# Performance work log

Hardware: AMD Instinct MI355X
Metric: run time of the kernel (lower is better)

## Reference

```python
import jax, jax.numpy as jnp
import numpy as np

N_NODES = 100000
N_EDGES = 1600000
F_IN = 128
HID = 128
N_CLASSES = 10
N_GRAPHS = 128
N_LAYERS = 4


def _uniform(key, shape, fan_in):
    s = 1.0 / np.sqrt(fan_in)
    return jax.random.uniform(key, shape, jnp.float32, -s, s)


def setup_inputs() -> dict:
    key = jax.random.key(0)
    ks = jax.random.split(key, 14)
    x = jax.random.normal(ks[0], (N_NODES, F_IN), jnp.float32)
    edge_index = jax.random.randint(ks[1], (2, N_EDGES), 0, N_NODES, dtype=jnp.int32)
    batch = jnp.sort(jax.random.randint(ks[2], (N_NODES,), 0, N_GRAPHS, dtype=jnp.int32))
    # GraphConv layer 1: lin_rel (with bias) + lin_root (no bias)
    W1_rel = _uniform(ks[3], (F_IN, HID), F_IN)
    b1_rel = _uniform(ks[4], (HID,), F_IN)
    W1_root = _uniform(ks[5], (F_IN, HID), F_IN)
    # remaining num_layers-1 GraphConv layers, stacked
    Wc_rel = _uniform(ks[6], (N_LAYERS - 1, HID, HID), HID)
    bc_rel = _uniform(ks[7], (N_LAYERS - 1, HID), HID)
    Wc_root = _uniform(ks[8], (N_LAYERS - 1, HID, HID), HID)
    # JumpingKnowledge 'cat' -> lin1: (num_layers*hidden) -> hidden
    Wl1 = _uniform(ks[9], (N_LAYERS * HID, HID), N_LAYERS * HID)
    bl1 = _uniform(ks[10], (HID,), N_LAYERS * HID)
    Wl2 = _uniform(ks[11], (HID, N_CLASSES), HID)
    bl2 = _uniform(ks[12], (N_CLASSES,), HID)
    return {
        "x": x, "edge_index": edge_index, "batch": batch,
        "W1_rel": W1_rel, "b1_rel": b1_rel, "W1_root": W1_root,
        "Wc_rel": Wc_rel, "bc_rel": bc_rel, "Wc_root": Wc_root,
        "Wl1": Wl1, "bl1": bl1, "Wl2": Wl2, "bl2": bl2,
    }


def reference(x, edge_index, batch, W1_rel, b1_rel, W1_root,
              Wc_rel, bc_rel, Wc_root, Wl1, bl1, Wl2, bl2):
    src, dst = edge_index[0], edge_index[1]

    def graph_conv(h, Wr, br, Wroot):
        # GraphConv (aggr='add'): lin_rel(sum_{j in N(i)} x_j) + lin_root(x_i)
        agg = jax.ops.segment_sum(h[src], dst, num_segments=N_NODES)
        return agg @ Wr + br + h @ Wroot

    counts = jax.ops.segment_sum(jnp.ones((N_NODES, 1), x.dtype), batch,
                                 num_segments=N_GRAPHS)
    counts = jnp.maximum(counts, 1.0)

    def global_mean_pool(h):
        sums = jax.ops.segment_sum(h, batch, num_segments=N_GRAPHS)
        return sums / counts

    h = jax.nn.relu(graph_conv(x, W1_rel, b1_rel, W1_root))
    xs = [global_mean_pool(h)]
    for i in range(N_LAYERS - 1):
        h = jax.nn.relu(graph_conv(h, Wc_rel[i], bc_rel[i], Wc_root[i]))
        xs.append(global_mean_pool(h))

    z = jnp.concatenate(xs, axis=-1)            # [N_GRAPHS, N_LAYERS*HID]
    z = jax.nn.relu(z @ Wl1 + bl1)
    return z @ Wl2 + bl2                        # [N_GRAPHS, N_CLASSES]
```

## Files before the change

### kernel.cpp

```cpp
#include <hip/hip_runtime.h>

#define NNODES 100000
#define NEDGES 1600000
#define FDIM 128
#define NGRAPHS 128
#define NLAYERS 4
#define NCLASS 10
#define LDC 136
#define LDC8 136
#define NBUCK 391
#define EBCAP 5120
#define EPB 4096
#define NBLK_E ((NEDGES + EPB - 1) / EPB)

typedef __attribute__((ext_vector_type(8))) short bf16x8;
typedef __attribute__((ext_vector_type(4))) float f32x4;
typedef __attribute__((ext_vector_type(2))) float f32x2;
typedef unsigned char u8;
typedef unsigned short u16;
typedef unsigned int u32;
typedef unsigned long long u64;

__device__ __forceinline__ u16 f2bf(float f) {
    u32 u = __float_as_uint(f);
    u += 0x7fffu + ((u >> 16) & 1u);
    return (u16)(u >> 16);
}
__device__ __forceinline__ u32 pack_bf(float a, float b) {
    return (u32)f2bf(a) | ((u32)f2bf(b) << 16);
}

__device__ __forceinline__ void gload_lds16(const u16* g, u16* l) {
    __builtin_amdgcn_global_load_lds(
        (const __attribute__((address_space(1))) u32*)g,
        (__attribute__((address_space(3))) u32*)l, 16, 0, 0);
}


__global__ __launch_bounds__(256) void conv_x(const float* __restrict__ x,
                                              u16* __restrict__ xb,
                                              u8* __restrict__ x8) {
    int i = (blockIdx.x * 256 + threadIdx.x) * 4;
    if (i < NNODES * FDIM) {
        float4 v = *(const float4*)(x + i);
        u32 p0 = pack_bf(v.x, v.y), p1 = pack_bf(v.z, v.w);
        *(u32*)(xb + i) = p0;
        *(u32*)(xb + i + 2) = p1;
        u32 a = (u32)__builtin_amdgcn_cvt_pk_fp8_f32(v.x, v.y, 0, 0);
        u32 b = (u32)__builtin_amdgcn_cvt_pk_fp8_f32(v.z, v.w, 0, 0);
        *(u32*)(x8 + i) = (a & 0xffffu) | (b << 16);
    }
}

__global__ __launch_bounds__(256) void conv_w(const float* __restrict__ W1_rel,
                                              const float* __restrict__ W1_root,
                                              const float* __restrict__ Wc_rel,
                                              const float* __restrict__ Wc_root,
                                              u16* __restrict__ Wcat) {
    int idx = blockIdx.x * 256 + threadIdx.x;
    if (idx >= NLAYERS * 256 * FDIM) return;
    int n = idx & 127;
    int k = (idx >> 7) & 255;
    int l = idx >> 15;
    const float* Wr = (l == 0) ? W1_rel  : Wc_rel  + (size_t)(l - 1) * FDIM * FDIM;
    const float* Wt = (l == 0) ? W1_root : Wc_root + (size_t)(l - 1) * FDIM * FDIM;
    float v = (k < 128) ? Wr[(size_t)k * FDIM + n] : Wt[(size_t)(k - 128) * FDIM + n];
    Wcat[(size_t)l * 32768 + (size_t)n * 256 + k] = f2bf(v);
}


__global__ __launch_bounds__(192) void graph_ptr_kernel(const int* __restrict__ batch,
                                                        int* __restrict__ gptr) {
    int g = threadIdx.x;
    if (g > NGRAPHS) return;
    int lo = 0, hi = NNODES;
    while (lo < hi) {
        int mid = (lo + hi) >> 1;
        if (batch[mid] < g) lo = mid + 1; else hi = mid;
    }
    gptr[g] = lo;
}

__global__ __launch_bounds__(256) void bcur_init(int* __restrict__ bcur) {
    int i = blockIdx.x * 256 + threadIdx.x;
    if (i < NBUCK) bcur[i] = i * EBCAP;
}

__global__ __launch_bounds__(256) void bucket_scatter(const int* __restrict__ src,
                                                      const int* __restrict__ dst,
                                                      int* __restrict__ bcur,
                                                      u64* __restrict__ ebuf) {
    __shared__ int cnt[NBUCK];
    for (int i = threadIdx.x; i < NBUCK; i += 256) cnt[i] = 0;
    __syncthreads();
    int e0 = blockIdx.x * EPB;
    int e1 = e0 + EPB; if (e1 > NEDGES) e1 = NEDGES;
    for (int e = e0 + threadIdx.x; e < e1; e += 256)
        atomicAdd(&cnt[dst[e] >> 8], 1);
    __syncthreads();
    for (int i = threadIdx.x; i < NBUCK; i += 256) {
        int c = cnt[i];
        if (c) cnt[i] = atomicAdd(&bcur[i], c);
    }
    __syncthreads();
    for (int e = e0 + threadIdx.x; e < e1; e += 256) {
        int d = dst[e], s = src[e];
        int pos = atomicAdd(&cnt[d >> 8], 1);
        ebuf[pos] = ((u64)(u32)d << 32) | (u32)s;
    }
}

__global__ __launch_bounds__(256) void bucket_csr(const u64* __restrict__ ebuf,
                                                  const int* __restrict__ bcur,
                                                  int* __restrict__ rowstart,
                                                  int* __restrict__ rowend,
                                                  int* __restrict__ csr) {
    __shared__ int cur[256];
    __shared__ int sd[256];
    int b = blockIdx.x, t = threadIdx.x;
    int ebase = b * EBCAP, eend = bcur[b];
    int n0 = b << 8;
    cur[t] = 0;
    __syncthreads();
    for (int e = ebase + t; e < eend; e += 256) {
        int d = (int)(ebuf[e] >> 32);
        atomicAdd(&cur[d & 255], 1);
    }
    __syncthreads();
    int v = cur[t];
    sd[t] = v;
    __syncthreads();
    for (int s = 1; s < 256; s <<= 1) {
        int add = (t >= s) ? sd[t - s] : 0;
        __syncthreads();
        sd[t] += add;
        __syncthreads();
    }
    int excl = sd[t] - v;
    cur[t] = ebase + excl;
    if (n0 + t < NNODES) {
        rowstart[n0 + t] = ebase + excl;
        rowend[n0 + t]   = ebase + excl + v;
    }
    __syncthreads();
    for (int e = ebase + t; e < eend; e += 256) {
        u64 r = ebuf[e];
        int d = (int)(r >> 32);
        int pos = atomicAdd(&cur[d & 255], 1);
        csr[pos] = (int)(r & 0xffffffffu);
    }
}


__global__ __launch_bounds__(256) void agg_bf(const u8* __restrict__ h8,
                                              const int* __restrict__ rowstart,
                                              const int* __restrict__ rowend,
                                              const int* __restrict__ csr,
                                              u16* __restrict__ agg) {
    int wave = threadIdx.x >> 6;
    int lane = threadIdx.x & 63;
    int node = (blockIdx.x << 2) + wave;
    if (node >= NNODES) return;
    int e0 = rowstart[node], e1 = rowend[node];
    int cnt = e1 - e0;
    float ax = 0.f, ay = 0.f;
    if (cnt <= 64) {
        int myidx = (lane < cnt) ? csr[e0 + lane] : 0;
        int nb = (cnt + 15) >> 4;
        for (int b = 0; b < nb; ++b) {
            int base = b * 16;
            u32 vv[16];
#pragma unroll
            for (int i = 0; i < 16; ++i) {
                int s = __builtin_amdgcn_readlane(myidx, base + i);
                vv[i] = *(const u16*)(h8 + (size_t)s * FDIM + lane * 2);
            }
            if (base + 16 <= cnt) {
#pragma unroll
                for (int i = 0; i < 16; ++i) {
                    f32x2 f = __builtin_amdgcn_cvt_pk_f32_fp8((int)vv[i], 0);
                    ax += f.x; ay += f.y;
                }
            } else {
#pragma unroll
                for (int i = 0; i < 16; ++i) {
                    f32x2 f = __builtin_amdgcn_cvt_pk_f32_fp8((int)vv[i], 0);
                    float m = (base + i < cnt) ? 1.f : 0.f;
                    ax = fmaf(f.x, m, ax);
                    ay = fmaf(f.y, m, ay);
                }
            }
        }
    } else {
        int e = e0;
        for (; e + 8 <= e1; e += 8) {
            u32 v0 = *(const u16*)(h8 + (size_t)csr[e]     * FDIM + lane * 2);
            u32 v1 = *(const u16*)(h8 + (size_t)csr[e + 1] * FDIM + lane * 2);
            u32 v2 = *(const u16*)(h8 + (size_t)csr[e + 2] * FDIM + lane * 2);
            u32 v3 = *(const u16*)(h8 + (size_t)csr[e + 3] * FDIM + lane * 2);
            u32 v4 = *(const u16*)(h8 + (size_t)csr[e + 4] * FDIM + lane * 2);
            u32 v5 = *(const u16*)(h8 + (size_t)csr[e + 5] * FDIM + lane * 2);
            u32 v6 = *(const u16*)(h8 + (size_t)csr[e + 6] * FDIM + lane * 2);
            u32 v7 = *(const u16*)(h8 + (size_t)csr[e + 7] * FDIM + lane * 2);
            f32x2 f0 = __builtin_amdgcn_cvt_pk_f32_fp8((int)v0, 0);
            f32x2 f1 = __builtin_amdgcn_cvt_pk_f32_fp8((int)v1, 0);
            f32x2 f2 = __builtin_amdgcn_cvt_pk_f32_fp8((int)v2, 0);
            f32x2 f3 = __builtin_amdgcn_cvt_pk_f32_fp8((int)v3, 0);
            f32x2 f4 = __builtin_amdgcn_cvt_pk_f32_fp8((int)v4, 0);
            f32x2 f5 = __builtin_amdgcn_cvt_pk_f32_fp8((int)v5, 0);
            f32x2 f6 = __builtin_amdgcn_cvt_pk_f32_fp8((int)v6, 0);
            f32x2 f7 = __builtin_amdgcn_cvt_pk_f32_fp8((int)v7, 0);
            ax += f0.x + f1.x + f2.x + f3.x + f4.x + f5.x + f6.x + f7.x;
            ay += f0.y + f1.y + f2.y + f3.y + f4.y + f5.y + f6.y + f7.y;
        }
        for (; e < e1; ++e) {
            u32 v0 = *(const u16*)(h8 + (size_t)csr[e] * FDIM + lane * 2);
            f32x2 f = __builtin_amdgcn_cvt_pk_f32_fp8((int)v0, 0);
            ax += f.x; ay += f.y;
        }
    }
    ((u32*)(agg + (size_t)node * FDIM))[lane] = pack_bf(ax, ay);
}


__global__ __launch_bounds__(256) void gemm_mfma(const u16* __restrict__ aggb,
                                                 const u16* __restrict__ hinb,
                                                 const u16* __restrict__ Wl,
                                                 const float* __restrict__ bias,
                                                 const int* __restrict__ batch,
                                                 float* __restrict__ z, int layer,
                                                 u16* __restrict__ houtb,
                                                 u8* __restrict__ hout8) {
    __shared__ u16 S[32768];
    __shared__ int batchs[128];
    u8* Cs8 = (u8*)S + 36864;
    const int t = threadIdx.x;
    const int lane = t & 63;
    const int w = t >> 6;
    const int wr = w >> 1, wc = w & 1;
    const int row0 = blockIdx.x * 128;
    const int lr = lane & 15;

    const int srow = lane >> 3;
    const int sq = lane & 7;

    auto STAGE = [&](int kb, u16* Abuf, u16* Bbuf) {
        const u16* xsrc = (kb < 2) ? aggb : hinb;
        const int koff = (kb & 1) * 64;
#pragma unroll
        for (int i = 0; i < 4; ++i) {
            int blk8 = w * 4 + i;
            int r = blk8 * 8 + srow;
            int sc = sq ^ (r & 7);
            int arow = row0 + r; if (arow > NNODES - 1) arow = NNODES - 1;
            gload_lds16(xsrc + (size_t)arow * FDIM + koff + sc * 8, Abuf + blk8 * 512);
            gload_lds16(Wl + (size_t)r * 256 + kb * 64 + sc * 8, Bbuf + blk8 * 512);
        }
    };

    f32x4 acc[4][4];
#pragma unroll
    for (int m = 0; m < 4; ++m)
#pragma unroll
        for (int n = 0; n < 4; ++n) acc[m][n] = (f32x4){0.f, 0.f, 0.f, 0.f};

    STAGE(0, S, S + 8192);
    if (t < 128) batchs[t] = (row0 + t < NNODES) ? batch[row0 + t] : NGRAPHS;
    __syncthreads();

    for (int kb = 0; kb < 4; ++kb) {
        u16* Ac = S + ((kb & 1) ? 16384 : 0);
        u16* Bc = Ac + 8192;
        if (kb < 3) {
            u16* An = S + ((kb & 1) ? 0 : 16384);
            STAGE(kb + 1, An, An + 8192);
        }
#pragma unroll
        for (int ks = 0; ks < 2; ++ks) {
            bf16x8 a[4], b[4];
            int qr = ks * 4 + (lane >> 4);
#pragma unroll
            for (int m = 0; m < 4; ++m) {
                int r = wr * 64 + m * 16 + lr;
                int ch = qr ^ (r & 7);
                a[m] = *(const bf16x8*)&Ac[r * 64 + ch * 8];
            }
#pragma unroll
            for (int n = 0; n < 4; ++n) {
                int r = wc * 64 + n * 16 + lr;
                int ch = qr ^ (r & 7);
                b[n] = *(const bf16x8*)&Bc[r * 64 + ch * 8];
            }
#pragma unroll
            for (int m = 0; m < 4; ++m)
#pragma unroll
                for (int n = 0; n < 4; ++n)
                    acc[m][n] = __builtin_amdgcn_mfma_f32_16x16x32_bf16(a[m], b[n], acc[m][n], 0, 0, 0);
        }
        __syncthreads();
    }
#pragma unroll
    for (int m = 0; m < 4; ++m) {
#pragma unroll
        for (int n = 0; n < 4; ++n) {
            int col = wc * 64 + n * 16 + lr;
            float bb = bias[col];
#pragma unroll
            for (int reg = 0; reg < 4; ++reg) {
                int row = wr * 64 + m * 16 + (lane >> 4) * 4 + reg;
                float v = fmaxf(acc[m][n][reg] + bb, 0.f);
                S[row * LDC + col] = f2bf(v);
                Cs8[row * LDC8 + col] = (u8)__builtin_amdgcn_cvt_pk_fp8_f32(v, v, 0, 0);
            }
        }
    }
    __syncthreads();
    {
        int r = t >> 1, half = t & 1;
        if (row0 + r < NNODES) {
#pragma unroll
            for (int j = 0; j < 8; ++j) {
                bf16x8 v = *(const bf16x8*)&S[r * LDC + half * 64 + j * 8];
                *(bf16x8*)(houtb + (size_t)(row0 + r) * FDIM + half * 64 + j * 8) = v;
            }
#pragma unroll
            for (int j = 0; j < 8; ++j) {
                u64 v8 = *(const u64*)&Cs8[r * LDC8 + half * 64 + j * 8];
                *(u64*)(hout8 + (size_t)(row0 + r) * FDIM + half * 64 + j * 8) = v8;
            }
        }
    }
    {
        int col = t & 127, half = t >> 7;
        int r0 = half * 64, r1 = r0 + 64;
        float* zl = z + (size_t)layer * FDIM + col;
        int g = batchs[r0];
        float s = 0.f;
        for (int r = r0; r < r1; ++r) {
            int gn = batchs[r];
            if (gn != g) {
                atomicAdd(zl + (size_t)g * (NLAYERS * FDIM), s);
                s = 0.f; g = gn;
            }
            s += __uint_as_float((u32)S[r * LDC + col] << 16);
        }
        atomicAdd(zl + (size_t)g * (NLAYERS * FDIM), s);
    }
}


__global__ __launch_bounds__(128) void mlp1(const float* __restrict__ z,
                                            const int* __restrict__ gptr,
                                            const float* __restrict__ Wl1,
                                            const float* __restrict__ bl1,
                                            float* __restrict__ z2) {
    int g = blockIdx.x, j = threadIdx.x;
    __shared__ float zs[NLAYERS * FDIM];
    int cnt = gptr[g + 1] - gptr[g]; if (cnt < 1) cnt = 1;
    float invc = 1.0f / (float)cnt;
    for (int k = j; k < NLAYERS * FDIM; k += 128)
        zs[k] = z[(size_t)g * (NLAYERS * FDIM) + k] * invc;
    __syncthreads();
    float s = bl1[j];
    for (int k = 0; k < NLAYERS * FDIM; ++k) s = fmaf(zs[k], Wl1[(size_t)k * FDIM + j], s);
    z2[(size_t)g * FDIM + j] = fmaxf(s, 0.f);
}

__global__ __launch_bounds__(128) void mlp2(const float* __restrict__ z2,
                                            const float* __restrict__ Wl2,
                                            const float* __restrict__ bl2,
                                            float* __restrict__ out) {
    int g = blockIdx.x, c = threadIdx.x;
    __shared__ float zs[FDIM];
    if (threadIdx.x < FDIM) zs[threadIdx.x] = z2[(size_t)g * FDIM + threadIdx.x];
    __syncthreads();
    if (c < NCLASS) {
        float s = bl2[c];
        for (int k = 0; k < FDIM; ++k) s = fmaf(zs[k], Wl2[(size_t)k * NCLASS + c], s);
        out[(size_t)g * NCLASS + c] = s;
    }
}


extern "C" void kernel_launch(void* const* d_in, const int* in_sizes, int n_in,
                              void* d_out, int out_size, void* d_ws, size_t ws_size,
                              hipStream_t stream) {
    const float* x       = (const float*)d_in[0];
    const int*   ei      = (const int*)d_in[1];
    const int*   batch   = (const int*)d_in[2];
    const float* W1_rel  = (const float*)d_in[3];
    const float* b1_rel  = (const float*)d_in[4];
    const float* W1_root = (const float*)d_in[5];
    const float* Wc_rel  = (const float*)d_in[6];
    const float* bc_rel  = (const float*)d_in[7];
    const float* Wc_root = (const float*)d_in[8];
    const float* Wl1     = (const float*)d_in[9];
    const float* bl1     = (const float*)d_in[10];
    const float* Wl2     = (const float*)d_in[11];
    const float* bl2     = (const float*)d_in[12];
    float* out = (float*)d_out;

    const int* srcv = ei;
    const int* dstv = ei + NEDGES;

    char* ws = (char*)d_ws;
    size_t off = 0;
    auto alloc = [&](size_t bytes) -> void* {
        void* p = ws + off;
        off = (off + bytes + 255) & ~(size_t)255;
        return p;
    };
    u16* xb      = (u16*)alloc((size_t)NNODES * FDIM * 2);
    u16* hA      = (u16*)alloc((size_t)NNODES * FDIM * 2);
    u16* hB      = (u16*)alloc((size_t)NNODES * FDIM * 2);
    u16* aggb    = (u16*)alloc((size_t)NNODES * FDIM * 2);
    u8*  x8      = (u8*)alloc((size_t)NNODES * FDIM);
    u8*  h8A     = (u8*)alloc((size_t)NNODES * FDIM);
    u8*  h8B     = (u8*)alloc((size_t)NNODES * FDIM);
    u16* Wcat    = (u16*)alloc((size_t)NLAYERS * 256 * FDIM * 2);
    int* csr     = (int*)alloc((size_t)NBUCK * EBCAP * 4);
    int* rowstart= (int*)alloc((size_t)NNODES * 4);
    int* rowend  = (int*)alloc((size_t)NNODES * 4);
    int* bcur    = (int*)alloc((size_t)(NBUCK + 1) * 4);
    int* gptr    = (int*)alloc(1024);
    float* z     = (float*)alloc((size_t)(NGRAPHS + 1) * NLAYERS * FDIM * 4);
    float* z2    = (float*)alloc((size_t)NGRAPHS * FDIM * 4);
    u64* ebuf    = (u64*)hA;
    (void)ws_size; (void)in_sizes; (void)n_in; (void)out_size;

    hipMemsetAsync(z, 0, (size_t)(NGRAPHS + 1) * NLAYERS * FDIM * 4, stream);
    conv_x<<<(NNODES * FDIM / 4 + 255) / 256, 256, 0, stream>>>(x, xb, x8);
    conv_w<<<(NLAYERS * 256 * FDIM + 255) / 256, 256, 0, stream>>>(W1_rel, W1_root, Wc_rel, Wc_root, Wcat);
    graph_ptr_kernel<<<1, 192, 0, stream>>>(batch, gptr);
    bcur_init<<<(NBUCK + 255) / 256, 256, 0, stream>>>(bcur);
    bucket_scatter<<<NBLK_E, 256, 0, stream>>>(srcv, dstv, bcur, ebuf);
    bucket_csr<<<NBUCK, 256, 0, stream>>>(ebuf, bcur, rowstart, rowend, csr);

    const u16* hin = xb;
    const u8*  hin8 = x8;
    for (int l = 0; l < NLAYERS; ++l) {
        u16* hout  = (l & 1) ? hB : hA;
        u8*  hout8 = (l & 1) ? h8B : h8A;
        const u16* Wl = Wcat + (size_t)l * 256 * FDIM;
        const float* bb = (l == 0) ? b1_rel : bc_rel + (size_t)(l - 1) * FDIM;
        agg_bf<<<(NNODES + 3) / 4, 256, 0, stream>>>(hin8, rowstart, rowend, csr, aggb);
        gemm_mfma<<<(NNODES + 127) / 128, 256, 0, stream>>>(aggb, hin, Wl, bb, batch, z, l, hout, hout8);
        hin = hout; hin8 = hout8;
    }
    mlp1<<<NGRAPHS, 128, 0, stream>>>(z, gptr, Wl1, bl1, z2);
    mlp2<<<NGRAPHS, 128, 0, stream>>>(z2, Wl2, bl2, out);
}
```

Before: 400.0 us.

## Aggregate two nodes per wave with 4-byte fp8 loads; single-buffer GEMM LDS

The neighbor aggregation kernel now gives each wave two destination nodes, one per 32-lane half. Each lane gathers 4 fp8 features with a 32-bit load and unpacks both halves, which halves the lanes spent per edge and widens each memory access. The fast path now needs both nodes to have at most 32 neighbors, and edge groups of 4 are masked by each half's own count. Separately, the MFMA GEMM drops its LDS double buffer for a single buffer with a sync after each stage, cutting shared-memory use to allow more resident blocks, at the cost of no longer overlapping loads with compute.

```diff
diff --git a/kernel.cpp b/kernel.cpp
--- a/kernel.cpp
+++ b/kernel.cpp
@@ -157,69 +157,73 @@
                                               const int* __restrict__ rowend,
                                               const int* __restrict__ csr,
                                               u16* __restrict__ agg) {
-    int wave = threadIdx.x >> 6;
-    int lane = threadIdx.x & 63;
-    int node = (blockIdx.x << 2) + wave;
-    if (node >= NNODES) return;
-    int e0 = rowstart[node], e1 = rowend[node];
-    int cnt = e1 - e0;
-    float ax = 0.f, ay = 0.f;
-    if (cnt <= 64) {
-        int myidx = (lane < cnt) ? csr[e0 + lane] : 0;
-        int nb = (cnt + 15) >> 4;
-        for (int b = 0; b < nb; ++b) {
-            int base = b * 16;
-            u32 vv[16];
-#pragma unroll
-            for (int i = 0; i < 16; ++i) {
-                int s = __builtin_amdgcn_readlane(myidx, base + i);
-                vv[i] = *(const u16*)(h8 + (size_t)s * FDIM + lane * 2);
-            }
-            if (base + 16 <= cnt) {
-#pragma unroll
-                for (int i = 0; i < 16; ++i) {
-                    f32x2 f = __builtin_amdgcn_cvt_pk_f32_fp8((int)vv[i], 0);
-                    ax += f.x; ay += f.y;
-                }
-            } else {
-#pragma unroll
-                for (int i = 0; i < 16; ++i) {
-                    f32x2 f = __builtin_amdgcn_cvt_pk_f32_fp8((int)vv[i], 0);
-                    float m = (base + i < cnt) ? 1.f : 0.f;
-                    ax = fmaf(f.x, m, ax);
-                    ay = fmaf(f.y, m, ay);
-                }
+    const int wid = threadIdx.x >> 6;
+    const int lane = threadIdx.x & 63;
+    const int half = lane >> 5;
+    const int sl = lane & 31;
+    const int pair = blockIdx.x * 4 + wid;
+    const int node = pair * 2 + half;
+    if (pair * 2 >= NNODES) return;
+
+    int e0 = rowstart[node];
+    int cnt = rowend[node] - e0;
+    float f0 = 0.f, f1 = 0.f, f2 = 0.f, f3 = 0.f;
+
+    int cA = __builtin_amdgcn_readlane(cnt, 0);
+    int cB = __builtin_amdgcn_readlane(cnt, 32);
+
+    if (cA <= 32 && cB <= 32) {
+        int myidx = (sl < cnt) ? csr[e0 + sl] : 0;
+        int cmin = cA < cB ? cA : cB;
+        int cmax = cA > cB ? cA : cB;
+        int bfull = cmin >> 2;
+        int btot = (cmax + 3) >> 2;
+        int b = 0;
+        for (; b < bfull; ++b) {
+            u32 v[4];
+#pragma unroll
+            for (int i = 0; i < 4; ++i) {
+                int iA = __builtin_amdgcn_readlane(myidx, b * 4 + i);
+                int iB = __builtin_amdgcn_readlane(myidx, 32 + b * 4 + i);
+                int s = half ? iB : iA;
+                v[i] = *(const u32*)(h8 + (size_t)s * FDIM + sl * 4);
+            }
+#pragma unroll
+            for (int i = 0; i < 4; ++i) {
+                f32x2 lo = __builtin_amdgcn_cvt_pk_f32_fp8((int)v[i], false);
+                f32x2 hi = __builtin_amdgcn_cvt_pk_f32_fp8((int)v[i], true);
+                f0 += lo.x; f1 += lo.y; f2 += hi.x; f3 += hi.y;
+            }
+        }
+        for (; b < btot; ++b) {
+            u32 v[4];
+#pragma unroll
+            for (int i = 0; i < 4; ++i) {
+                int iA = __builtin_amdgcn_readlane(myidx, b * 4 + i);
+                int iB = __builtin_amdgcn_readlane(myidx, 32 + b * 4 + i);
+                int s = half ? iB : iA;
+                v[i] = *(const u32*)(h8 + (size_t)s * FDIM + sl * 4);
+            }
+#pragma unroll
+            for (int i = 0; i < 4; ++i) {
+                float m = (b * 4 + i < cnt) ? 1.f : 0.f;
+                f32x2 lo = __builtin_amdgcn_cvt_pk_f32_fp8((int)v[i], false);
+                f32x2 hi = __builtin_amdgcn_cvt_pk_f32_fp8((int)v[i], true);
+                f0 = fmaf(lo.x, m, f0); f1 = fmaf(lo.y, m, f1);
+                f2 = fmaf(hi.x, m, f2); f3 = fmaf(hi.y, m, f3);
             }
         }
     } else {
-        int e = e0;
-        for (; e + 8 <= e1; e += 8) {
-            u32 v0 = *(const u16*)(h8 + (size_t)csr[e]     * FDIM + lane * 2);
-            u32 v1 = *(const u16*)(h8 + (size_t)csr[e + 1] * FDIM + lane * 2);
-            u32 v2 = *(const u16*)(h8 + (size_t)csr[e + 2] * FDIM + lane * 2);
-            u32 v3 = *(const u16*)(h8 + (size_t)csr[e + 3] * FDIM + lane * 2);
-            u32 v4 = *(const u16*)(h8 + (size_t)csr[e + 4] * FDIM + lane * 2);
-            u32 v5 = *(const u16*)(h8 + (size_t)csr[e + 5] * FDIM + lane * 2);
-            u32 v6 = *(const u16*)(h8 + (size_t)csr[e + 6] * FDIM + lane * 2);
-            u32 v7 = *(const u16*)(h8 + (size_t)csr[e + 7] * FDIM + lane * 2);
-            f32x2 f0 = __builtin_amdgcn_cvt_pk_f32_fp8((int)v0, 0);
-            f32x2 f1 = __builtin_amdgcn_cvt_pk_f32_fp8((int)v1, 0);
-            f32x2 f2 = __builtin_amdgcn_cvt_pk_f32_fp8((int)v2, 0);
-            f32x2 f3 = __builtin_amdgcn_cvt_pk_f32_fp8((int)v3, 0);
-            f32x2 f4 = __builtin_amdgcn_cvt_pk_f32_fp8((int)v4, 0);
-            f32x2 f5 = __builtin_amdgcn_cvt_pk_f32_fp8((int)v5, 0);
-            f32x2 f6 = __builtin_amdgcn_cvt_pk_f32_fp8((int)v6, 0);
-            f32x2 f7 = __builtin_amdgcn_cvt_pk_f32_fp8((int)v7, 0);
-            ax += f0.x + f1.x + f2.x + f3.x + f4.x + f5.x + f6.x + f7.x;
-            ay += f0.y + f1.y + f2.y + f3.y + f4.y + f5.y + f6.y + f7.y;
-        }
-        for (; e < e1; ++e) {
-            u32 v0 = *(const u16*)(h8 + (size_t)csr[e] * FDIM + lane * 2);
-            f32x2 f = __builtin_amdgcn_cvt_pk_f32_fp8((int)v0, 0);
-            ax += f.x; ay += f.y;
-        }
-    }
-    ((u32*)(agg + (size_t)node * FDIM))[lane] = pack_bf(ax, ay);
+        for (int e = 0; e < cnt; ++e) {
+            int s = csr[e0 + e];
+            u32 v = *(const u32*)(h8 + (size_t)s * FDIM + sl * 4);
+            f32x2 lo = __builtin_amdgcn_cvt_pk_f32_fp8((int)v, false);
+            f32x2 hi = __builtin_amdgcn_cvt_pk_f32_fp8((int)v, true);
+            f0 += lo.x; f1 += lo.y; f2 += hi.x; f3 += hi.y;
+        }
+    }
+    u32 p0 = pack_bf(f0, f1), p1 = pack_bf(f2, f3);
+    *(u64*)(agg + (size_t)node * FDIM + sl * 4) = ((u64)p1 << 32) | (u64)p0;
 }
 
 
@@ -231,9 +235,11 @@
                                                  float* __restrict__ z, int layer,
                                                  u16* __restrict__ houtb,
                                                  u8* __restrict__ hout8) {
-    __shared__ u16 S[32768];
+    __shared__ u16 S[26112];
     __shared__ int batchs[128];
-    u8* Cs8 = (u8*)S + 36864;
+    u16* As = S;
+    u16* Bs = S + 8192;
+    u8* Cs8 = (u8*)S + 34816;
     const int t = threadIdx.x;
     const int lane = t & 63;
     const int w = t >> 6;
@@ -244,7 +250,15 @@
     const int srow = lane >> 3;
     const int sq = lane & 7;
 
-    auto STAGE = [&](int kb, u16* Abuf, u16* Bbuf) {
+    f32x4 acc[4][4];
+#pragma unroll
+    for (int m = 0; m < 4; ++m)
+#pragma unroll
+        for (int n = 0; n < 4; ++n) acc[m][n] = (f32x4){0.f, 0.f, 0.f, 0.f};
+
+    if (t < 128) batchs[t] = (row0 + t < NNODES) ? batch[row0 + t] : NGRAPHS;
+
+    for (int kb = 0; kb < 4; ++kb) {
         const u16* xsrc = (kb < 2) ? aggb : hinb;
         const int koff = (kb & 1) * 64;
 #pragma unroll
@@ -253,28 +267,10 @@
             int r = blk8 * 8 + srow;
             int sc = sq ^ (r & 7);
             int arow = row0 + r; if (arow > NNODES - 1) arow = NNODES - 1;
-            gload_lds16(xsrc + (size_t)arow * FDIM + koff + sc * 8, Abuf + blk8 * 512);
-            gload_lds16(Wl + (size_t)r * 256 + kb * 64 + sc * 8, Bbuf + blk8 * 512);
-        }
-    };
-
-    f32x4 acc[4][4];
-#pragma unroll
-    for (int m = 0; m < 4; ++m)
-#pragma unroll
-        for (int n = 0; n < 4; ++n) acc[m][n] = (f32x4){0.f, 0.f, 0.f, 0.f};
-
-    STAGE(0, S, S + 8192);
-    if (t < 128) batchs[t] = (row0 + t < NNODES) ? batch[row0 + t] : NGRAPHS;
-    __syncthreads();
-
-    for (int kb = 0; kb < 4; ++kb) {
-        u16* Ac = S + ((kb & 1) ? 16384 : 0);
-        u16* Bc = Ac + 8192;
-        if (kb < 3) {
-            u16* An = S + ((kb & 1) ? 0 : 16384);
-            STAGE(kb + 1, An, An + 8192);
-        }
+            gload_lds16(xsrc + (size_t)arow * FDIM + koff + sc * 8, As + blk8 * 512);
+            gload_lds16(Wl + (size_t)r * 256 + kb * 64 + sc * 8, Bs + blk8 * 512);
+        }
+        __syncthreads();
 #pragma unroll
         for (int ks = 0; ks < 2; ++ks) {
             bf16x8 a[4], b[4];
@@ -283,13 +279,13 @@
             for (int m = 0; m < 4; ++m) {
                 int r = wr * 64 + m * 16 + lr;
                 int ch = qr ^ (r & 7);
-                a[m] = *(const bf16x8*)&Ac[r * 64 + ch * 8];
+                a[m] = *(const bf16x8*)&As[r * 64 + ch * 8];
             }
 #pragma unroll
             for (int n = 0; n < 4; ++n) {
                 int r = wc * 64 + n * 16 + lr;
                 int ch = qr ^ (r & 7);
-                b[n] = *(const bf16x8*)&Bc[r * 64 + ch * 8];
+                b[n] = *(const bf16x8*)&Bs[r * 64 + ch * 8];
             }
 #pragma unroll
             for (int m = 0; m < 4; ++m)
@@ -438,12 +434,13 @@
 
     const u16* hin = xb;
     const u8*  hin8 = x8;
+    const int npairs = NNODES / 2;
     for (int l = 0; l < NLAYERS; ++l) {
         u16* hout  = (l & 1) ? hB : hA;
         u8*  hout8 = (l & 1) ? h8B : h8A;
         const u16* Wl = Wcat + (size_t)l * 256 * FDIM;
         const float* bb = (l == 0) ? b1_rel : bc_rel + (size_t)(l - 1) * FDIM;
-        agg_bf<<<(NNODES + 3) / 4, 256, 0, stream>>>(hin8, rowstart, rowend, csr, aggb);
+        agg_bf<<<(npairs + 3) / 4, 256, 0, stream>>>(hin8, rowstart, rowend, csr, aggb);
         gemm_mfma<<<(NNODES + 127) / 128, 256, 0, stream>>>(aggb, hin, Wl, bb, batch, z, l, hout, hout8);
         hin = hout; hin8 = hout8;
     }
```

New measurement: 389.1 us. 2.7% less time.
